# Kernel tuning notes

Measured on AMD Instinct MI355X. Metric: run time of the kernel, lower is better.

The kernel has to match this reference:

```python
import jax, jax.numpy as jnp
import numpy as np

B, S, D = 1, 2048, 4096
H, KVH, DH = 32, 8, 128          # nheads, kv heads, head dim (GQA expansion = 4)
HID = 11008                       # 256 * ceil(4096 * (8/3) / 256)
EPS = 1e-5
ROPE_BASE = 10000.0


def setup_inputs() -> dict:
    key = jax.random.key(0)
    ks = jax.random.split(key, 10)
    std = 0.02
    w = lambda k, shape: jax.random.normal(k, shape, dtype=jnp.float32) * std
    return {
        "x": jax.random.normal(ks[0], (B, S, D), dtype=jnp.float32),
        "position_ids": jnp.broadcast_to(jnp.arange(S, dtype=jnp.int32), (B, S)),
        "ln_w": jnp.ones((D,), dtype=jnp.float32),
        "ffln_w": jnp.ones((D,), dtype=jnp.float32),
        "wq": w(ks[1], (D, H * DH)),
        "wk": w(ks[2], (D, KVH * DH)),
        "wv": w(ks[3], (D, KVH * DH)),
        "wo": w(ks[4], (H * DH, D)),
        "wg": w(ks[5], (D, HID)),
        "w1": w(ks[6], (D, HID)),
        "w2": w(ks[7], (HID, D)),
    }


def rmsnorm(x, w, eps=EPS):
    # LayerNormParameterized(use_mean=False, use_high_precision_pow=True)
    xf = x.astype(jnp.float32)
    var = jnp.mean(xf * xf, axis=-1, keepdims=True)
    return (xf * jax.lax.rsqrt(var + eps)).astype(x.dtype) * w


def rope(x, pos):
    # interleaved (complex-pair) rotary embedding; x: [B,S,h,DH], pos: [B,S]
    dh = x.shape[-1]
    inv_freq = 1.0 / (ROPE_BASE ** (jnp.arange(0, dh, 2, dtype=jnp.float32) / dh))
    ang = pos.astype(jnp.float32)[:, :, None, None] * inv_freq  # [B,S,1,dh/2]
    cos, sin = jnp.cos(ang), jnp.sin(ang)
    x1, x2 = x[..., 0::2], x[..., 1::2]
    return jnp.stack([x1 * cos - x2 * sin, x1 * sin + x2 * cos], axis=-1).reshape(x.shape)


def block(x, position_ids, ln_w, ffln_w, wq, wk, wv, wo, wg, w1, w2):
    # --- attention sublayer ---
    a = rmsnorm(x, ln_w)
    q = (a @ wq).reshape(B, S, H, DH)
    k = (a @ wk).reshape(B, S, KVH, DH)
    v = (a @ wv).reshape(B, S, KVH, DH)
    q = rope(q, position_ids)
    k = rope(k, position_ids)
    # GQA expansion: kv head g serves query heads [g*exp, (g+1)*exp)
    exp = H // KVH
    k_e = jnp.repeat(k, exp, axis=2)  # [B,S,H,DH]
    v_e = jnp.repeat(v, exp, axis=2)
    scores = jnp.einsum("bqhd,bkhd->bhqk", q, k_e) / np.sqrt(DH).astype(np.float32)
    causal = jnp.tril(jnp.ones((S, S), dtype=bool))
    scores = jnp.where(causal, scores, jnp.finfo(scores.dtype).min)
    p = jax.nn.softmax(scores, axis=-1)
    attn = jnp.einsum("bhqk,bkhd->bqhd", p, v_e).reshape(B, S, H * DH)
    x = x + attn @ wo
    # --- SwiGLU FFN sublayer ---
    b = rmsnorm(x, ffln_w)
    ff = (jax.nn.silu(b @ wg) * (b @ w1)) @ w2
    return x + ff


def reference(x, position_ids, ln_w, ffln_w, wq, wk, wv, wo, wg, w1, w2):
    return block(x, position_ids, ln_w, ffln_w, wq, wk, wv, wo, wg, w1, w2)
```

## Files before the change

kernel.cpp:

```cpp
#include <hip/hip_runtime.h>
#include <hip/hip_bf16.h>

typedef __bf16 bf16_t;
typedef __bf16 bf16x4 __attribute__((ext_vector_type(4)));
typedef __bf16 bf16x8 __attribute__((ext_vector_type(8)));
typedef float f32x4 __attribute__((ext_vector_type(4)));

#define S_ 2048
#define D_ 4096
#define H_ 32
#define KVH_ 8
#define DH_ 128
#define HID_ 11008
#define QKV_N 6144
#define GU_N 22016

__device__ __forceinline__ void gl16(const bf16_t* g, bf16_t* l) {
  __builtin_amdgcn_global_load_lds(
      (const __attribute__((address_space(1))) unsigned int*)g,
      (__attribute__((address_space(3))) unsigned int*)l, 16, 0, 0);
}

#define VMW(N)                                          \
  asm volatile("s_waitcnt vmcnt(" #N ")" ::: "memory"); \
  __builtin_amdgcn_sched_barrier(0)

#define BAR()                          \
  asm volatile("" ::: "memory");       \
  __builtin_amdgcn_s_barrier();        \
  asm volatile("" ::: "memory")

__global__ __launch_bounds__(256) void rmsnorm_kernel(
    const float* __restrict__ x, const float* __restrict__ w,
    bf16_t* __restrict__ out) {
  int row = blockIdx.x;
  const float* xr = x + (size_t)row * D_;
  float ss = 0.f;
  #pragma unroll
  for (int it = 0; it < 4; ++it) {
    int i = threadIdx.x * 4 + it * 1024;
    float4 v = *(const float4*)(xr + i);
    ss += v.x * v.x + v.y * v.y + v.z * v.z + v.w * v.w;
  }
  #pragma unroll
  for (int off = 32; off; off >>= 1) ss += __shfl_xor(ss, off);
  __shared__ float s4[4];
  if ((threadIdx.x & 63) == 0) s4[threadIdx.x >> 6] = ss;
  __syncthreads();
  float tot = s4[0] + s4[1] + s4[2] + s4[3];
  float rinv = rsqrtf(tot / (float)D_ + 1e-5f);
  bf16_t* orow = out + (size_t)row * D_;
  #pragma unroll
  for (int it = 0; it < 4; ++it) {
    int i = threadIdx.x * 4 + it * 1024;
    float4 v = *(const float4*)(xr + i);
    orow[i + 0] = (bf16_t)(v.x * rinv * w[i + 0]);
    orow[i + 1] = (bf16_t)(v.y * rinv * w[i + 1]);
    orow[i + 2] = (bf16_t)(v.z * rinv * w[i + 2]);
    orow[i + 3] = (bf16_t)(v.w * rinv * w[i + 3]);
  }
}

__global__ __launch_bounds__(256) void combine_rms_kernel(
    const float* __restrict__ x, const float* __restrict__ p0,
    const float* __restrict__ p1, const float* __restrict__ w,
    float* __restrict__ x1, bf16_t* __restrict__ out) {
  int row = blockIdx.x;
  size_t base = (size_t)row * D_;
  float ss = 0.f;
  float4 vals[4];
  #pragma unroll
  for (int it = 0; it < 4; ++it) {
    int i = threadIdx.x * 4 + it * 1024;
    float4 a = *(const float4*)(x + base + i);
    float4 b = *(const float4*)(p0 + base + i);
    float4 c = *(const float4*)(p1 + base + i);
    float4 v;
    v.x = a.x + b.x + c.x; v.y = a.y + b.y + c.y;
    v.z = a.z + b.z + c.z; v.w = a.w + b.w + c.w;
    vals[it] = v;
    *(float4*)(x1 + base + i) = v;
    ss += v.x * v.x + v.y * v.y + v.z * v.z + v.w * v.w;
  }
  #pragma unroll
  for (int off = 32; off; off >>= 1) ss += __shfl_xor(ss, off);
  __shared__ float s4[4];
  if ((threadIdx.x & 63) == 0) s4[threadIdx.x >> 6] = ss;
  __syncthreads();
  float tot = s4[0] + s4[1] + s4[2] + s4[3];
  float rinv = rsqrtf(tot / (float)D_ + 1e-5f);
  #pragma unroll
  for (int it = 0; it < 4; ++it) {
    int i = threadIdx.x * 4 + it * 1024;
    float4 v = vals[it];
    out[base + i + 0] = (bf16_t)(v.x * rinv * w[i + 0]);
    out[base + i + 1] = (bf16_t)(v.y * rinv * w[i + 1]);
    out[base + i + 2] = (bf16_t)(v.z * rinv * w[i + 2]);
    out[base + i + 3] = (bf16_t)(v.w * rinv * w[i + 3]);
  }
}

__global__ __launch_bounds__(256) void combine_out_kernel(
    const float* __restrict__ x1, const float* __restrict__ p0,
    const float* __restrict__ p1, float* __restrict__ outp) {
  size_t i = ((size_t)blockIdx.x * 256 + threadIdx.x) * 4;
  float4 a = *(const float4*)(x1 + i);
  float4 b = *(const float4*)(p0 + i);
  float4 c = *(const float4*)(p1 + i);
  float4 v;
  v.x = a.x + b.x + c.x; v.y = a.y + b.y + c.y;
  v.z = a.z + b.z + c.z; v.w = a.w + b.w + c.w;
  *(float4*)(outp + i) = v;
}

__global__ __launch_bounds__(256) void wtrans_kernel(
    const float* __restrict__ W, bf16_t* __restrict__ WT, int K, int N) {
  __shared__ bf16_t t[32][258];
  int k0 = blockIdx.x * 32, n0 = blockIdx.y * 256;
  #pragma unroll
  for (int i = 0; i < 8; ++i) {
    int flat = i * 1024 + threadIdx.x * 4;
    int kk = flat >> 8, nn = flat & 255;
    float4 wv = *(const float4*)(W + (size_t)(k0 + kk) * N + n0 + nn);
    bf16_t* p = &t[kk][nn];
    p[0] = (bf16_t)wv.x; p[1] = (bf16_t)wv.y;
    p[2] = (bf16_t)wv.z; p[3] = (bf16_t)wv.w;
  }
  __syncthreads();
  int kc8 = (threadIdx.x & 3) * 8;
  #pragma unroll
  for (int i = 0; i < 4; ++i) {
    int nn = i * 64 + (threadIdx.x >> 2);
    bf16x8 vals;
    #pragma unroll
    for (int j = 0; j < 8; ++j) vals[j] = t[kc8 + j][nn];
    *(bf16x8*)(WT + (size_t)(n0 + nn) * K + k0 + kc8) = vals;
  }
}

__global__ __launch_bounds__(256) void vtrans_kernel(
    const bf16_t* __restrict__ qkv, bf16_t* __restrict__ vt) {
  __shared__ bf16_t t[64][72];
  int s0 = blockIdx.x * 64, d0 = blockIdx.y * 64;
  #pragma unroll
  for (int it = 0; it < 2; ++it) {
    int r = (threadIdx.x >> 3) + it * 32;
    int c = (threadIdx.x & 7) * 8;
    *(bf16x8*)&t[r][c] =
        *(const bf16x8*)(qkv + (size_t)(s0 + r) * QKV_N + 5120 + d0 + c);
  }
  __syncthreads();
  #pragma unroll
  for (int it = 0; it < 2; ++it) {
    int c = threadIdx.x & 63;
    int sb = (threadIdx.x >> 6) * 16 + it * 8;
    bf16x8 v;
    #pragma unroll
    for (int j = 0; j < 8; ++j) v[j] = t[sb + j][c];
    *(bf16x8*)(vt + (size_t)(d0 + c) * S_ + s0 + sb) = v;
  }
}

__global__ __launch_bounds__(256) void rope_table_kernel(
    const int* __restrict__ pos_ids, float* __restrict__ cos_t,
    float* __restrict__ sin_t) {
  int idx = blockIdx.x * 256 + threadIdx.x;
  int s = idx >> 6, i = idx & 63;
  float pos = (float)pos_ids[s];
  float inv_freq = exp2f(-(float)i * (13.287712379549449f / 64.0f));
  float ang = pos * inv_freq;
  cos_t[idx] = cosf(ang);
  sin_t[idx] = sinf(ang);
}

__global__ __launch_bounds__(256) void rope_kernel(
    bf16_t* __restrict__ buf, const float* __restrict__ cos_t,
    const float* __restrict__ sin_t, int nheads, int colbase, int total) {
  int idx = blockIdx.x * 256 + threadIdx.x;
  if (idx >= total) return;
  int i = idx & 63;
  int t2 = idx >> 6;
  int s = t2 / nheads, h = t2 % nheads;
  size_t base = (size_t)s * QKV_N + colbase + h * 128 + 2 * i;
  float x1 = (float)buf[base], x2 = (float)buf[base + 1];
  float c = cos_t[s * 64 + i], sn = sin_t[s * 64 + i];
  buf[base]     = (bf16_t)(x1 * c - x2 * sn);
  buf[base + 1] = (bf16_t)(x1 * sn + x2 * c);
}

#define DO_PHASE(BI, KK, MH, DO_LDB, STAGE1, STAGE2, WAITCODE)             \
  {                                                                        \
    _Pragma("unroll") for (int m = 0; m < 4; ++m)                          \
      aF[m] = *(const bf16x8*)&lds[BI][0][wr][KK]                          \
          [((MH) * 64 + m * 16 + fr) * 32 + rc * 8];                       \
    if (DO_LDB) {                                                          \
      _Pragma("unroll") for (int n = 0; n < 4; ++n)                        \
        bF[n] = *(const bf16x8*)&lds[BI][1][wcH][KK]                       \
            [(wcL * 64 + n * 16 + fr) * 32 + rc * 8];                      \
    }                                                                      \
    STAGE1;                                                                \
    STAGE2;                                                                \
    asm volatile("" ::: "memory");                                         \
    __builtin_amdgcn_s_barrier();                                          \
    asm volatile("s_waitcnt lgkmcnt(0)" ::: "memory");                     \
    __builtin_amdgcn_sched_barrier(0);                                     \
    __builtin_amdgcn_s_setprio(1);                                         \
    _Pragma("unroll") for (int m = 0; m < 4; ++m)                          \
      _Pragma("unroll") for (int n = 0; n < 4; ++n)                        \
        acc[(MH) * 4 + m][n] = __builtin_amdgcn_mfma_f32_16x16x32_bf16(    \
            aF[m], bF[n], acc[(MH) * 4 + m][n], 0, 0, 0);                  \
    __builtin_amdgcn_s_setprio(0);                                         \
    __builtin_amdgcn_sched_barrier(0);                                     \
    WAITCODE;                                                              \
    asm volatile("" ::: "memory");                                         \
    __builtin_amdgcn_s_barrier();                                          \
    asm volatile("" ::: "memory");                                         \
  }

#define DO_TILE(BI, T)                                                     \
  {                                                                        \
    const int Tp1 = (T) + 1 < NT, Tp2 = (T) + 2 < NT;                      \
    DO_PHASE(BI, 0, 0, 1,                                                  \
             if (Tp1) stage(BI ^ 1, 0, 0, 1, (T) + 1),                     \
             if (Tp1) stage(BI ^ 1, 1, 0, 1, (T) + 1), );                  \
    DO_PHASE(BI, 0, 1, 0,                                                  \
             if (Tp1) stage(BI ^ 1, 0, 1, 1, (T) + 1),                     \
             if (Tp1) stage(BI ^ 1, 1, 1, 1, (T) + 1),                     \
             if (Tp1) { VMW(8); } else { VMW(0); });                       \
    DO_PHASE(BI, 1, 0, 1,                                                  \
             if (Tp2) stage(BI, 0, 0, 0, (T) + 2),                         \
             if (Tp2) stage(BI, 1, 0, 0, (T) + 2), );                      \
    DO_PHASE(BI, 1, 1, 0,                                                  \
             if (Tp2) stage(BI, 0, 1, 0, (T) + 2),                         \
             if (Tp2) stage(BI, 1, 1, 0, (T) + 2),                         \
             if (Tp2) { VMW(8); } else if (Tp1) { VMW(4); });              \
  }

template <int MODE, int SPLIT>
__global__ __launch_bounds__(512, 2) void gemm256_kernel(
    const bf16_t* __restrict__ A, int lda, const bf16_t* __restrict__ BT,
    int ldb, void* __restrict__ Cout, int ldc, int K) {
  __shared__ __align__(16) bf16_t lds[2][2][2][2][128 * 32];

  const int tid = threadIdx.x;
  const int lane = tid & 63;
  const int wid = tid >> 6;
  const int wr = wid >> 2;
  const int wc = wid & 3;
  const int wcH = wc >> 1, wcL = wc & 1;
  const int g = lane >> 4, fr = lane & 15;
  const int rc = (g + ((fr >> 1) & 3)) & 3;

  const int nwg = gridDim.x;
  const int orig = blockIdx.x;
  int wg = (orig & 7) * (nwg >> 3) + (orig >> 3);
  int kz = 0;
  if constexpr (SPLIT) {
    const int half = nwg >> 1;
    kz = wg >= half;
    wg -= kz * half;
  }
  const int bx = wg & 7;
  const int by = wg >> 3;
  const size_t row0 = (size_t)bx * 256, col0 = (size_t)by * 256;

  const int srow = tid >> 2;
  const int schunk = ((tid & 3) - ((tid >> 3) & 3)) & 3;

  const size_t lda2 = (size_t)lda * 2, ldb2 = (size_t)ldb * 2;
  const size_t kzoff = (size_t)kz * K * 2;
  const char* aB0 =
      (const char*)A + (row0 + srow) * lda2 + schunk * 16 + kzoff;
  const char* aB1 = aB0 + (size_t)128 * lda2;
  const char* bB0 =
      (const char*)BT + (col0 + srow) * ldb2 + schunk * 16 + kzoff;
  const char* bB1 = bB0 + (size_t)128 * ldb2;

  auto stage = [&](int bi, int ab, int h, int kk, int kt) {
    const char* base = ab ? (h ? bB1 : bB0) : (h ? aB1 : aB0);
    gl16((const bf16_t*)(base + (size_t)kt * 128 + kk * 64),
         &lds[bi][ab][h][kk][tid * 8]);
  };

  f32x4 acc[8][4] = {};
  bf16x8 aF[4], bF[4];
  const int NT = K / 64;

  stage(0, 0, 0, 0, 0); stage(0, 1, 0, 0, 0);
  stage(0, 0, 1, 0, 0); stage(0, 1, 1, 0, 0);
  stage(0, 0, 0, 1, 0); stage(0, 1, 0, 1, 0);
  stage(0, 0, 1, 1, 0); stage(0, 1, 1, 1, 0);
  stage(1, 0, 0, 0, 1); stage(1, 1, 0, 0, 1);
  stage(1, 0, 1, 0, 1); stage(1, 1, 1, 0, 1);
  VMW(4);
  BAR();

  for (int T = 0; T < NT; T += 2) {
    DO_TILE(0, T);
    DO_TILE(1, T + 1);
  }

  float* fOut = (float*)Cout + (size_t)kz * 2048 * ldc;
  #pragma unroll
  for (int mf = 0; mf < 8; ++mf)
    #pragma unroll
    for (int n = 0; n < 4; ++n)
      #pragma unroll
      for (int r = 0; r < 4; ++r) {
        size_t row = row0 + wr * 128 + mf * 16 + g * 4 + r;
        size_t col = col0 + wc * 64 + n * 16 + fr;
        float val = acc[mf][n][r];
        if constexpr (MODE == 0) {
          ((bf16_t*)Cout)[row * ldc + col] = (bf16_t)val;
        } else {
          fOut[row * ldc + col] = val;
        }
      }
}

__global__ __launch_bounds__(256, 2) void attn_kernel(
    const bf16_t* __restrict__ qkv, const bf16_t* __restrict__ vt,
    bf16_t* __restrict__ o) {
  int h = blockIdx.y;
  int qb = (S_ / 64 - 1) - blockIdx.x;
  int kvh = h >> 2;
  int tid = threadIdx.x;
  int wid = tid >> 6, lane = tid & 63;
  int g = lane >> 4, fr = lane & 15;

  __shared__ __align__(16) bf16_t kfl[2][8192];
  __shared__ __align__(16) bf16_t vfl[2][8192];
  __shared__ __align__(16) bf16_t p_lds[4][16][72];

  const int fr_s = (tid >> 2) & 15, g_s = tid & 3;
  const int kcw = (tid >> 6) & 3;
  const int kc2w = (tid >> 6) & 1;
  const int nhi = tid >> 7;
  const bf16_t* kSrc = qkv + (size_t)fr_s * QKV_N + 4096 + kvh * 128 +
                       (kcw * 4 + g_s) * 8;
  const bf16_t* vSrc = vt + ((size_t)kvh * 128 + nhi * 16 + fr_s) * S_ +
                       (kc2w * 4 + g_s) * 8;

  auto stage = [&](int bi, int t) {
    size_t kv0 = (size_t)t * 64;
    #pragma unroll
    for (int i = 0; i < 4; ++i)
      gl16(kSrc + (kv0 + i * 16) * QKV_N, &kfl[bi][(i * 256 + tid) * 8]);
    #pragma unroll
    for (int i = 0; i < 4; ++i)
      gl16(vSrc + (size_t)i * 32 * S_ + kv0, &vfl[bi][(i * 256 + tid) * 8]);
  };

  int q0w = qb * 64 + wid * 16;
  bf16x8 q_frag[4];
  const bf16_t* qptr = qkv + (size_t)(q0w + fr) * QKV_N + h * 128;
  #pragma unroll
  for (int kc = 0; kc < 4; ++kc)
    q_frag[kc] = *(const bf16x8*)(qptr + kc * 32 + g * 8);
  VMW(0);

  stage(0, 0);

  f32x4 o_frag[8] = {};
  float m_run[4], l_run[4];
  #pragma unroll
  for (int r = 0; r < 4; ++r) { m_run[r] = -1e30f; l_run[r] = 0.f; }

  const float sc = 0.08838834764831845f * 1.4426950408889634f;

  for (int t = 0; t <= qb; ++t) {
    int cur = t & 1;
    int kv0 = t * 64;
    if (t < qb) {
      stage(cur ^ 1, t + 1);
      VMW(8);
    } else {
      VMW(0);
    }
    BAR();

    f32x4 sfr[4];
    #pragma unroll
    for (int nf = 0; nf < 4; ++nf) {
      f32x4 acc = {};
      #pragma unroll
      for (int kc = 0; kc < 4; ++kc) {
        bf16x8 kf =
            *(const bf16x8*)&kfl[cur][(nf * 256 + kc * 64 + fr * 4 + g) * 8];
        acc = __builtin_amdgcn_mfma_f32_16x16x32_bf16(q_frag[kc], kf, acc, 0, 0, 0);
      }
      sfr[nf] = acc;
    }

    bool diag = (t == qb);
    float mtile[4];
    #pragma unroll
    for (int r = 0; r < 4; ++r) mtile[r] = -1e30f;
    #pragma unroll
    for (int nf = 0; nf < 4; ++nf)
      #pragma unroll
      for (int r = 0; r < 4; ++r) {
        if (diag) {
          int kvg = kv0 + nf * 16 + fr;
          int qg = q0w + 4 * g + r;
          if (kvg > qg) sfr[nf][r] = -1e30f;
        }
        mtile[r] = fmaxf(mtile[r], sfr[nf][r]);
      }
    #pragma unroll
    for (int r = 0; r < 4; ++r) {
      float mv = mtile[r];
      mv = fmaxf(mv, __shfl_xor(mv, 1));
      mv = fmaxf(mv, __shfl_xor(mv, 2));
      mv = fmaxf(mv, __shfl_xor(mv, 4));
      mv = fmaxf(mv, __shfl_xor(mv, 8));
      mtile[r] = mv;
    }
    float alpha[4];
    #pragma unroll
    for (int r = 0; r < 4; ++r) {
      float m_new = fmaxf(m_run[r], mtile[r]);
      alpha[r] = exp2f((m_run[r] - m_new) * sc);
      m_run[r] = m_new;
    }
    float lsum[4] = {0.f, 0.f, 0.f, 0.f};
    #pragma unroll
    for (int nf = 0; nf < 4; ++nf)
      #pragma unroll
      for (int r = 0; r < 4; ++r) {
        float p = exp2f((sfr[nf][r] - m_run[r]) * sc);
        sfr[nf][r] = p;
        lsum[r] += p;
      }
    #pragma unroll
    for (int r = 0; r < 4; ++r) {
      float lv = lsum[r];
      lv += __shfl_xor(lv, 1);
      lv += __shfl_xor(lv, 2);
      lv += __shfl_xor(lv, 4);
      lv += __shfl_xor(lv, 8);
      l_run[r] = l_run[r] * alpha[r] + lv;
    }
    #pragma unroll
    for (int nfo = 0; nfo < 8; ++nfo)
      #pragma unroll
      for (int r = 0; r < 4; ++r) o_frag[nfo][r] *= alpha[r];

    #pragma unroll
    for (int nf = 0; nf < 4; ++nf)
      #pragma unroll
      for (int r = 0; r < 4; ++r)
        p_lds[wid][4 * g + r][nf * 16 + fr] = (bf16_t)sfr[nf][r];

    #pragma unroll
    for (int kc2 = 0; kc2 < 2; ++kc2) {
      bf16x8 pf = *(const bf16x8*)&p_lds[wid][fr][kc2 * 32 + g * 8];
      #pragma unroll
      for (int nfo = 0; nfo < 8; ++nfo) {
        bf16x8 vf =
            *(const bf16x8*)&vfl[cur][(nfo * 128 + kc2 * 64 + fr * 4 + g) * 8];
        o_frag[nfo] = __builtin_amdgcn_mfma_f32_16x16x32_bf16(pf, vf, o_frag[nfo], 0, 0, 0);
      }
    }
    BAR();
  }

  #pragma unroll
  for (int nfo = 0; nfo < 8; ++nfo)
    #pragma unroll
    for (int r = 0; r < 4; ++r) {
      int qg = q0w + 4 * g + r;
      float val = o_frag[nfo][r] / l_run[r];
      o[(size_t)qg * (H_ * DH_) + h * DH_ + nfo * 16 + fr] = (bf16_t)val;
    }
}

__global__ __launch_bounds__(256) void silu_mul_kernel(bf16_t* __restrict__ gu) {
  size_t idx = (size_t)blockIdx.x * 256 + threadIdx.x;
  int r = (int)(idx / (HID_ / 8));
  int c8 = (int)(idx % (HID_ / 8));
  bf16_t* p = gu + (size_t)r * GU_N + c8 * 8;
  bf16x8 g8 = *(const bf16x8*)p;
  bf16x8 u8 = *(const bf16x8*)(p + HID_);
  bf16x8 h8;
  #pragma unroll
  for (int j = 0; j < 8; ++j) {
    float gv = (float)g8[j];
    float uv = (float)u8[j];
    h8[j] = (bf16_t)(gv / (1.f + __expf(-gv)) * uv);
  }
  *(bf16x8*)p = h8;
}

extern "C" void kernel_launch(void* const* d_in, const int* in_sizes, int n_in,
                              void* d_out, int out_size, void* d_ws,
                              size_t ws_size, hipStream_t stream) {
  const float* x = (const float*)d_in[0];
  const int* pos = (const int*)d_in[1];
  const float* ln_w = (const float*)d_in[2];
  const float* ffln_w = (const float*)d_in[3];
  const float* wq = (const float*)d_in[4];
  const float* wk = (const float*)d_in[5];
  const float* wv = (const float*)d_in[6];
  const float* wo = (const float*)d_in[7];
  const float* wg = (const float*)d_in[8];
  const float* w1 = (const float*)d_in[9];
  const float* w2 = (const float*)d_in[10];

  char* ws = (char*)d_ws;
  size_t off = 0;
  auto alloc = [&](size_t bytes) {
    size_t o = off;
    off = (off + bytes + 255) & ~(size_t)255;
    return o;
  };
  bf16_t* Wbuf = (bf16_t*)(ws + alloc((size_t)GU_N * D_ * 2));
  bf16_t* nbuf = (bf16_t*)(ws + alloc((size_t)S_ * D_ * 2));
  bf16_t* qkv  = (bf16_t*)(ws + alloc((size_t)S_ * QKV_N * 2));
  float*  x1   = (float*)(ws + alloc((size_t)S_ * D_ * 4));
  bf16_t* gu   = (bf16_t*)(ws + alloc((size_t)S_ * GU_N * 2));
  bf16_t* vtb  = (bf16_t*)(ws + alloc((size_t)KVH_ * DH_ * S_ * 2));
  float*  cos_t = (float*)(ws + alloc((size_t)S_ * 64 * 4));
  float*  sin_t = (float*)(ws + alloc((size_t)S_ * 64 * 4));
  float* part = (float*)((char*)Wbuf + ((size_t)96 << 20));

  rmsnorm_kernel<<<S_, 256, 0, stream>>>(x, ln_w, nbuf);
  wtrans_kernel<<<dim3(D_ / 32, D_ / 256), 256, 0, stream>>>(wq, Wbuf, D_, D_);
  wtrans_kernel<<<dim3(D_ / 32, 1024 / 256), 256, 0, stream>>>(
      wk, Wbuf + (size_t)4096 * D_, D_, 1024);
  wtrans_kernel<<<dim3(D_ / 32, 1024 / 256), 256, 0, stream>>>(
      wv, Wbuf + (size_t)5120 * D_, D_, 1024);
  rope_table_kernel<<<(S_ * 64) / 256, 256, 0, stream>>>(pos, cos_t, sin_t);
  gemm256_kernel<0, 0><<<dim3((S_ / 256) * (QKV_N / 256)), 512, 0, stream>>>(
      nbuf, D_, Wbuf, D_, qkv, QKV_N, D_);
  rope_kernel<<<(S_ * H_ * 64) / 256, 256, 0, stream>>>(
      qkv, cos_t, sin_t, H_, 0, S_ * H_ * 64);
  rope_kernel<<<(S_ * KVH_ * 64) / 256, 256, 0, stream>>>(
      qkv, cos_t, sin_t, KVH_, 4096, S_ * KVH_ * 64);
  vtrans_kernel<<<dim3(S_ / 64, (KVH_ * DH_) / 64), 256, 0, stream>>>(qkv, vtb);
  attn_kernel<<<dim3(S_ / 64, H_), 256, 0, stream>>>(qkv, vtb, nbuf);
  wtrans_kernel<<<dim3(D_ / 32, D_ / 256), 256, 0, stream>>>(wo, Wbuf, D_, D_);
  gemm256_kernel<2, 1><<<dim3((S_ / 256) * (D_ / 256) * 2), 512, 0, stream>>>(
      nbuf, D_, Wbuf, D_, part, D_, 2048);
  combine_rms_kernel<<<S_, 256, 0, stream>>>(
      x, part, part + (size_t)S_ * D_, ffln_w, x1, nbuf);
  wtrans_kernel<<<dim3(D_ / 32, HID_ / 256), 256, 0, stream>>>(wg, Wbuf, D_, HID_);
  wtrans_kernel<<<dim3(D_ / 32, HID_ / 256), 256, 0, stream>>>(
      w1, Wbuf + (size_t)HID_ * D_, D_, HID_);
  gemm256_kernel<0, 0><<<dim3((S_ / 256) * (GU_N / 256)), 512, 0, stream>>>(
      nbuf, D_, Wbuf, D_, gu, GU_N, D_);
  silu_mul_kernel<<<(S_ * HID_ / 8) / 256, 256, 0, stream>>>(gu);
  wtrans_kernel<<<dim3(HID_ / 32, D_ / 256), 256, 0, stream>>>(w2, Wbuf, HID_, D_);
  gemm256_kernel<2, 1><<<dim3((S_ / 256) * (D_ / 256) * 2), 512, 0, stream>>>(
      gu, GU_N, Wbuf, HID_, part, D_, 5504);
  combine_out_kernel<<<(S_ * D_ / 4) / 256, 256, 0, stream>>>(
      x1, part, part + (size_t)S_ * D_, (float*)d_out);
}
```

Baseline: 1.195 ms.

## Double-buffer LDS fragment registers to overlap reads with MFMA in GEMM

Restructures the GEMM main loop so the LDS fragment reads for the next phase go into a second register set while the current phase's MFMAs run. Partial lgkmcnt waits replace full drains, and the wait on global loads moves before the final phase's staging. The aim is to hide LDS read latency behind matrix math instead of stalling before each MFMA block. In exchange the kernel uses more VGPRs for the extra fragment sets, and the hand-tuned waitcnt counts and barrier placement carry a risk of races or wrong results.

```diff
diff --git a/kernel.cpp b/kernel.cpp
--- a/kernel.cpp
+++ b/kernel.cpp
@@ -23,6 +23,10 @@
 
 #define VMW(N)                                          \
   asm volatile("s_waitcnt vmcnt(" #N ")" ::: "memory"); \
+  __builtin_amdgcn_sched_barrier(0)
+
+#define LGKM(N)                                           \
+  asm volatile("s_waitcnt lgkmcnt(" #N ")" ::: "memory"); \
   __builtin_amdgcn_sched_barrier(0)
 
 #define BAR()                          \
@@ -188,52 +192,58 @@
   buf[base + 1] = (bf16_t)(x1 * sn + x2 * c);
 }
 
-#define DO_PHASE(BI, KK, MH, DO_LDB, STAGE1, STAGE2, WAITCODE)             \
-  {                                                                        \
-    _Pragma("unroll") for (int m = 0; m < 4; ++m)                          \
-      aF[m] = *(const bf16x8*)&lds[BI][0][wr][KK]                          \
-          [((MH) * 64 + m * 16 + fr) * 32 + rc * 8];                       \
-    if (DO_LDB) {                                                          \
-      _Pragma("unroll") for (int n = 0; n < 4; ++n)                        \
-        bF[n] = *(const bf16x8*)&lds[BI][1][wcH][KK]                       \
-            [(wcL * 64 + n * 16 + fr) * 32 + rc * 8];                      \
-    }                                                                      \
-    STAGE1;                                                                \
-    STAGE2;                                                                \
-    asm volatile("" ::: "memory");                                         \
-    __builtin_amdgcn_s_barrier();                                          \
-    asm volatile("s_waitcnt lgkmcnt(0)" ::: "memory");                     \
-    __builtin_amdgcn_sched_barrier(0);                                     \
-    __builtin_amdgcn_s_setprio(1);                                         \
-    _Pragma("unroll") for (int m = 0; m < 4; ++m)                          \
-      _Pragma("unroll") for (int n = 0; n < 4; ++n)                        \
-        acc[(MH) * 4 + m][n] = __builtin_amdgcn_mfma_f32_16x16x32_bf16(    \
-            aF[m], bF[n], acc[(MH) * 4 + m][n], 0, 0, 0);                  \
-    __builtin_amdgcn_s_setprio(0);                                         \
-    __builtin_amdgcn_sched_barrier(0);                                     \
-    WAITCODE;                                                              \
-    asm volatile("" ::: "memory");                                         \
-    __builtin_amdgcn_s_barrier();                                          \
-    asm volatile("" ::: "memory");                                         \
-  }
+
+#define READ_A(dst, BIx, KK, MH)                                           \
+  _Pragma("unroll") for (int m = 0; m < 4; ++m)                            \
+    dst[m] = *(const bf16x8*)&lds[BIx][0][wr][KK]                          \
+        [((MH) * 64 + m * 16 + fr) * 32 + rc * 8];
+
+#define READ_B(dst, BIx, KK)                                               \
+  _Pragma("unroll") for (int n = 0; n < 4; ++n)                            \
+    dst[n] = *(const bf16x8*)&lds[BIx][1][wcH][KK]                         \
+        [(wcL * 64 + n * 16 + fr) * 32 + rc * 8];
+
+#define MFMA16(aS, bS, MH)                                                 \
+  __builtin_amdgcn_s_setprio(1);                                           \
+  _Pragma("unroll") for (int m = 0; m < 4; ++m)                            \
+    _Pragma("unroll") for (int n = 0; n < 4; ++n)                          \
+      acc[(MH) * 4 + m][n] = __builtin_amdgcn_mfma_f32_16x16x32_bf16(      \
+          aS[m], bS[n], acc[(MH) * 4 + m][n], 0, 0, 0);                    \
+  __builtin_amdgcn_s_setprio(0);
 
 #define DO_TILE(BI, T)                                                     \
   {                                                                        \
     const int Tp1 = (T) + 1 < NT, Tp2 = (T) + 2 < NT;                      \
-    DO_PHASE(BI, 0, 0, 1,                                                  \
-             if (Tp1) stage(BI ^ 1, 0, 0, 1, (T) + 1),                     \
-             if (Tp1) stage(BI ^ 1, 1, 0, 1, (T) + 1), );                  \
-    DO_PHASE(BI, 0, 1, 0,                                                  \
-             if (Tp1) stage(BI ^ 1, 0, 1, 1, (T) + 1),                     \
-             if (Tp1) stage(BI ^ 1, 1, 1, 1, (T) + 1),                     \
-             if (Tp1) { VMW(8); } else { VMW(0); });                       \
-    DO_PHASE(BI, 1, 0, 1,                                                  \
-             if (Tp2) stage(BI, 0, 0, 0, (T) + 2),                         \
-             if (Tp2) stage(BI, 1, 0, 0, (T) + 2), );                      \
-    DO_PHASE(BI, 1, 1, 0,                                                  \
-             if (Tp2) stage(BI, 0, 1, 0, (T) + 2),                         \
-             if (Tp2) stage(BI, 1, 1, 0, (T) + 2),                         \
-             if (Tp2) { VMW(8); } else if (Tp1) { VMW(4); });              \
+                    \
+    READ_A(aR1, BI, 0, 1);                                                 \
+    if (Tp1) { stage(BI ^ 1, 0, 0, 1, (T) + 1);                            \
+               stage(BI ^ 1, 1, 0, 1, (T) + 1); }                          \
+    BAR(); LGKM(4);                                                        \
+    MFMA16(aR0, bR0, 0);                                                   \
+    BAR();                                                                 \
+        \
+    READ_A(aR0, BI, 1, 0);                                                 \
+    READ_B(bR1, BI, 1);                                                    \
+    if (Tp1) { stage(BI ^ 1, 0, 1, 1, (T) + 1);                            \
+               stage(BI ^ 1, 1, 1, 1, (T) + 1); }                          \
+    BAR(); LGKM(8);                                                        \
+    MFMA16(aR1, bR0, 1);                                                   \
+    BAR();                                                                 \
+                    \
+    READ_A(aR1, BI, 1, 1);                                                 \
+    if (Tp2) { stage(BI, 0, 0, 0, (T) + 2);                                \
+               stage(BI, 1, 0, 0, (T) + 2); }                              \
+    BAR(); LGKM(4);                                                        \
+    MFMA16(aR0, bR1, 0);                                                   \
+    BAR();                                                                 \
+    \
+    if (Tp2) { VMW(2); } else if (Tp1) { VMW(0); }                         \
+    if (Tp2) { stage(BI, 0, 1, 0, (T) + 2);                                \
+               stage(BI, 1, 1, 0, (T) + 2); }                              \
+    BAR(); LGKM(0);                                                        \
+    if (Tp1) { READ_A(aR0, BI ^ 1, 0, 0); READ_B(bR0, BI ^ 1, 0); }        \
+    MFMA16(aR1, bR1, 1);                                                   \
+    BAR();                                                                 \
   }
 
 template <int MODE, int SPLIT>
@@ -283,7 +293,7 @@
   };
 
   f32x4 acc[8][4] = {};
-  bf16x8 aF[4], bF[4];
+  bf16x8 aR0[4], aR1[4], bR0[4], bR1[4];
   const int NT = K / 64;
 
   stage(0, 0, 0, 0, 0); stage(0, 1, 0, 0, 0);
@@ -294,6 +304,8 @@
   stage(1, 0, 1, 0, 1); stage(1, 1, 1, 0, 1);
   VMW(4);
   BAR();
+  READ_A(aR0, 0, 0, 0);
+  READ_B(bR0, 0, 0);
 
   for (int T = 0; T < NT; T += 2) {
     DO_TILE(0, T);
```

New measurement: 2.169 ms. 1.82x slower.
